# Kernel tuning notes

Measured on AMD Instinct MI355X. Metric: run time of the kernel, lower is better.

Reference implementation:

```python
import jax, jax.numpy as jnp
import numpy as np

HEADS = 8

def group_conv1x1(x, w, heads):
    # x: (B, Cin, H, W); w: (Cout, Cin//heads, 1, 1) grouped 1x1 conv, no bias
    B, Cin, H, W = x.shape
    Cout = w.shape[0]
    xg = x.reshape(B, heads, Cin // heads, H * W)
    wg = w[:, :, 0, 0].reshape(heads, Cout // heads, Cin // heads)
    out = jnp.einsum('hoc,bhcl->bhol', wg, xg)
    return out.reshape(B, Cout, H, W)

def sine_pe(d_model, length):
    # standard transformer sin/cos encoding, laid out as (d_model, length)
    pos = jnp.arange(length, dtype=jnp.float32)
    i = jnp.arange(0, d_model, 2, dtype=jnp.float32)
    div = jnp.exp(-(jnp.log(10000.0)) * i / d_model)
    ang = div[:, None] * pos[None, :]            # (d/2, L)
    pe = jnp.zeros((d_model, length), dtype=jnp.float32)
    pe = pe.at[0::2].set(jnp.sin(ang)).at[1::2].set(jnp.cos(ang))
    return pe

def setup_inputs() -> dict:
    key = jax.random.key(0)
    k0, k1, k2, k3 = jax.random.split(key, 4)
    B, Cin, H, W = 16, 256, 32, 32
    Cout, heads = 256, HEADS
    fan_out = Cout  # kaiming_normal fan_out for 1x1 conv = Cout*1*1
    std = np.sqrt(2.0 / fan_out)
    x = jax.random.normal(k0, (B, Cin, H, W), dtype=jnp.float32)
    wq = jax.random.normal(k1, (Cout, Cin // heads, 1, 1), dtype=jnp.float32) * std
    wk = jax.random.normal(k2, (Cout, Cin // heads, 1, 1), dtype=jnp.float32) * std
    wv = jax.random.normal(k3, (Cout, Cin // heads, 1, 1), dtype=jnp.float32) * std
    return {"x": x, "wq": wq, "wk": wk, "wv": wv}

def reference(x, wq, wk, wv):
    B, Cin, H, W = x.shape
    Cout = wq.shape[0]
    heads = HEADS
    dh = Cout // heads
    L = H * W

    q = group_conv1x1(x, wq, heads)              # (B, Cout, H, W)
    k = group_conv1x1(x, wk, heads)
    v = group_conv1x1(x, wv, heads)

    # sine positional encoding added to keys over flattened spatial positions
    k = k.reshape(B, Cout, L) + sine_pe(Cout, L)[None]

    q = q.reshape(B, heads, dh, L)               # (B, h, dh, L)
    k = k.reshape(B, heads, dh, L)
    v = v.reshape(B, heads, dh, L)

    scores = jnp.einsum('bhdq,bhdk->bhqk', q, k)  # (B, h, L, L) -- no sqrt(d) scaling, as in source
    attn = jax.nn.softmax(scores, axis=-1)
    out = jnp.einsum('bhqk,bhdk->bhdq', attn, v)  # (B, h, dh, L)
    return out.reshape(B, Cout, H, W)
```

## Files before the change

kernel.cpp:

```cpp
#include <hip/hip_runtime.h>

#define LL   1024
#define BHD  128
#define LOG2E 1.44269504088896340736f

typedef unsigned int       uint;
typedef unsigned short     ushort;
typedef unsigned long long ull;

typedef __attribute__((ext_vector_type(8)))  __bf16          bf16x8;
typedef __attribute__((ext_vector_type(8)))  unsigned short  u16x8;
typedef __attribute__((ext_vector_type(2)))  uint            ui32x2;
typedef __attribute__((ext_vector_type(4)))  uint            ui32x4;
typedef __attribute__((ext_vector_type(4)))  float           f32x4;
typedef __attribute__((ext_vector_type(16))) float           f32x16;

static __device__ __forceinline__ ushort f2bf(float f){
  union {float f; uint u;} v; v.f = f;
  uint u = v.u + 0x7fffu + ((v.u >> 16) & 1u);
  return (ushort)(u >> 16);
}
static __device__ __forceinline__ uint pack2(float a, float b){
  return (uint)f2bf(a) | ((uint)f2bf(b) << 16);
}
static __device__ __forceinline__ uint packtrunc(float a, float b){
  union {float f; uint u;} x, y; x.f = a; y.f = b;
  return __builtin_amdgcn_perm(y.u, x.u, 0x07060302u);
}
static __device__ __forceinline__ bf16x8 ld_frag(const ushort* p){
  u16x8 t = *(const u16x8*)p;
  return __builtin_bit_cast(bf16x8, t);
}

static __device__ __forceinline__ bool sniff_is_bf16(const uint* xw, int tid, int* cnt){
  uint w = xw[tid & 255];
  uint e = (w >> 7) & 0xFFu;
  bool hit = (e >= 118u) && (e <= 132u);
  ull b = __ballot(hit);
  if ((tid & 63) == 0) cnt[tid >> 6] = __popcll(b);
  __syncthreads();
  bool r = (cnt[0] + cnt[1] + cnt[2] + cnt[3]) > 128;
  __syncthreads();
  return r;
}

__global__ __launch_bounds__(256) void qkv_kernel(
    const void* __restrict__ xr,
    const void* __restrict__ wqr,
    const void* __restrict__ wkr,
    const void* __restrict__ wvr,
    ushort* __restrict__ Qt, ushort* __restrict__ Kt, ushort* __restrict__ Vt)
{
  const int bh   = blockIdx.x;
  const int lt   = blockIdx.y;
  const int tid  = threadIdx.x;
  const int wave = tid >> 6;
  const int lane = tid & 63;
  const int l16  = lane & 15;
  const int quad = lane >> 4;
  const int lbase = lt * 128;

  __shared__ int cnt[4];
  __shared__ __align__(16) uint xsd[128][20];

  const bool is_bf = sniff_is_bf16((const uint*)xr, tid, cnt);

  {
    const int cp = tid & 15, lg = tid >> 4;
    const size_t rb = (size_t)(bh*32 + 2*cp)*LL + lbase + lg*8;
    uint dw[8];
    if (is_bf){
      u16x8 e = *(const u16x8*)((const ushort*)xr + rb);
      u16x8 o = *(const u16x8*)((const ushort*)xr + rb + LL);
      #pragma unroll
      for (int j = 0; j < 8; ++j) dw[j] = (uint)e[j] | ((uint)o[j] << 16);
    } else {
      const float* xf = (const float*)xr;
      float4 e0 = *(const float4*)(xf + rb);
      float4 e1 = *(const float4*)(xf + rb + 4);
      float4 o0 = *(const float4*)(xf + rb + LL);
      float4 o1 = *(const float4*)(xf + rb + LL + 4);
      dw[0]=pack2(e0.x,o0.x); dw[1]=pack2(e0.y,o0.y);
      dw[2]=pack2(e0.z,o0.z); dw[3]=pack2(e0.w,o0.w);
      dw[4]=pack2(e1.x,o1.x); dw[5]=pack2(e1.y,o1.y);
      dw[6]=pack2(e1.z,o1.z); dw[7]=pack2(e1.w,o1.w);
    }
    #pragma unroll
    for (int j = 0; j < 8; ++j) xsd[lg*8 + j][cp] = dw[j];
  }
  __syncthreads();

  const void* wsrc[3] = {wqr, wkr, wvr};
  bf16x8 bw[3][2];
  #pragma unroll
  for (int p = 0; p < 3; ++p)
    #pragma unroll
    for (int nh = 0; nh < 2; ++nh){
      const int row = (bh & 7)*32 + nh*16 + l16;
      if (is_bf){
        bw[p][nh] = ld_frag((const ushort*)wsrc[p] + (size_t)row*32 + quad*8);
      } else {
        const float* wf = (const float*)wsrc[p] + (size_t)row*32 + quad*8;
        float4 f0 = *(const float4*)wf, f1 = *(const float4*)(wf + 4);
        u16x8 t;
        t[0]=f2bf(f0.x); t[1]=f2bf(f0.y); t[2]=f2bf(f0.z); t[3]=f2bf(f0.w);
        t[4]=f2bf(f1.x); t[5]=f2bf(f1.y); t[6]=f2bf(f1.z); t[7]=f2bf(f1.w);
        bw[p][nh] = __builtin_bit_cast(bf16x8, t);
      }
    }

  bf16x8 ax[2];
  #pragma unroll
  for (int mt = 0; mt < 2; ++mt)
    ax[mt] = __builtin_bit_cast(bf16x8,
               *(const ui32x4*)&xsd[wave*32 + mt*16 + l16][quad*4]);

  const f32x4 z = {0.f,0.f,0.f,0.f};
  f32x4 dq[2][2], dk[2][2], dv[2][2];
  #pragma unroll
  for (int nh = 0; nh < 2; ++nh)
    #pragma unroll
    for (int mt = 0; mt < 2; ++mt){
      dq[nh][mt] = __builtin_amdgcn_mfma_f32_16x16x32_bf16(bw[0][nh], ax[mt], z, 0,0,0);
      dk[nh][mt] = __builtin_amdgcn_mfma_f32_16x16x32_bf16(bw[1][nh], ax[mt], z, 0,0,0);
      dv[mt][nh] = __builtin_amdgcn_mfma_f32_16x16x32_bf16(ax[mt], bw[2][nh], z, 0,0,0);
    }

  const int kt2   = lt*2 + (wave >> 1);
  const size_t bhb = (size_t)bh * 32768;

  #pragma unroll
  for (int nh = 0; nh < 2; ++nh)
    #pragma unroll
    for (int mt = 0; mt < 2; ++mt){
      const int l  = lbase + wave*32 + mt*16 + l16;
      const int d0 = nh*16 + quad*4;
      ui32x2 ww = { pack2(dq[nh][mt][0], dq[nh][mt][1]),
                    pack2(dq[nh][mt][2], dq[nh][mt][3]) };
      *(ui32x2*)&Qt[((size_t)bh*LL + l)*32 + d0] = ww;
    }

  #pragma unroll
  for (int nh = 0; nh < 2; ++nh)
    #pragma unroll
    for (int mt = 0; mt < 2; ++mt){
      const int l  = lbase + wave*32 + mt*16 + l16;
      const int d0 = nh*16 + quad*4;
      const int c0 = (bh & 7)*32 + d0;
      const float fa = __expf(-0.03597789207f * (float)c0);
      const float fb = __expf(-0.03597789207f * (float)(c0 + 2));
      const float aa = fa * (float)l, ab = fb * (float)l;
      const float k0 = (dk[nh][mt][0] + __sinf(aa)) * LOG2E;
      const float k1 = (dk[nh][mt][1] + __cosf(aa)) * LOG2E;
      const float k2 = (dk[nh][mt][2] + __sinf(ab)) * LOG2E;
      const float k3 = (dk[nh][mt][3] + __cosf(ab)) * LOG2E;
      const size_t off = bhb + (size_t)kt2*2048 + (size_t)(wave & 1)*1024
                       + (size_t)nh*512 + (size_t)(quad >> 1)*256
                       + (size_t)(mt*16 + l16)*8 + (quad & 1)*4;
      ui32x2 ww = { pack2(k0, k1), pack2(k2, k3) };
      *(ui32x2*)&Kt[off] = ww;
    }

  #pragma unroll
  for (int mt = 0; mt < 2; ++mt)
    #pragma unroll
    for (int dh = 0; dh < 2; ++dh){
      const size_t off = bhb + (size_t)kt2*2048 + (size_t)((wave*2 + mt) & 3)*512
                       + (size_t)(quad >> 1)*256 + (size_t)(dh*16 + l16)*8
                       + (quad & 1)*4;
      ui32x2 ww = { pack2(dv[mt][dh][0], dv[mt][dh][1]),
                    pack2(dv[mt][dh][2], dv[mt][dh][3]) };
      *(ui32x2*)&Vt[off] = ww;
    }
}

__global__ __launch_bounds__(256, 4) void attn_kernel(
    const void*   __restrict__ xr,
    const ushort* __restrict__ Qt,
    const ushort* __restrict__ Kt,
    const ushort* __restrict__ Vt,
    void* __restrict__ out)
{
  const int bh  = blockIdx.x;
  const int qt  = blockIdx.y;
  const int tid = threadIdx.x;
  const int wave = tid >> 6;
  const int lane = tid & 63;
  const int q32  = lane & 31;
  const int h    = lane >> 5;

  __shared__ int cnt[4];
  const bool is_bf = sniff_is_bf16((const uint*)xr, tid, cnt);

  const int qg = qt*128 + wave*32 + q32;
  const ushort* qrow = Qt + ((size_t)bh*LL + qg)*32;
  bf16x8 bq0 = ld_frag(qrow + h*8);
  bf16x8 bq1 = ld_frag(qrow + 16 + h*8);

  const ushort* kb = Kt + (size_t)bh*32768 + h*256 + q32*8;
  const ushort* vb = Vt + (size_t)bh*32768 + h*256 + q32*8;

  f32x16 O = {};
  float rsum = 0.f;

  for (int kt = 0; kt < 16; ++kt){
    const ushort* kp = kb + kt*2048;
    const ushort* vp = vb + kt*2048;
    bf16x8 k00 = ld_frag(kp);
    bf16x8 k01 = ld_frag(kp + 512);
    bf16x8 k10 = ld_frag(kp + 1024);
    bf16x8 k11 = ld_frag(kp + 1536);
    bf16x8 vf[4];
    vf[0] = ld_frag(vp);
    vf[1] = ld_frag(vp + 512);
    vf[2] = ld_frag(vp + 1024);
    vf[3] = ld_frag(vp + 1536);

    f32x16 st[2];
    { f32x16 zz = {};
      st[0] = __builtin_amdgcn_mfma_f32_32x32x16_bf16(k00, bq0, zz,    0,0,0);
      st[0] = __builtin_amdgcn_mfma_f32_32x32x16_bf16(k01, bq1, st[0], 0,0,0);
      st[1] = __builtin_amdgcn_mfma_f32_32x32x16_bf16(k10, bq0, zz,    0,0,0);
      st[1] = __builtin_amdgcn_mfma_f32_32x32x16_bf16(k11, bq1, st[1], 0,0,0); }

    uint pr[2][8];
    #pragma unroll
    for (int t = 0; t < 2; ++t){
      float ts = 0.f;
      #pragma unroll
      for (int zi = 0; zi < 8; ++zi){
        float p0 = __builtin_amdgcn_exp2f(st[t][2*zi]);
        float p1 = __builtin_amdgcn_exp2f(st[t][2*zi+1]);
        ts += p0 + p1;
        pr[t][zi] = packtrunc(p0, p1);
      }
      rsum += ts;
    }

    #pragma unroll
    for (int c = 0; c < 4; ++c){
      const int t = c >> 1, g0 = 4*(c & 1);
      uint s0 = h ? pr[t][g0+0] : pr[t][g0+2];
      uint s1 = h ? pr[t][g0+1] : pr[t][g0+3];
      uint r0 = (uint)__shfl_xor((int)s0, 32);
      uint r1 = (uint)__shfl_xor((int)s1, 32);
      ui32x4 pb;
      pb[0] = h ? r0 : pr[t][g0+0];
      pb[1] = h ? r1 : pr[t][g0+1];
      pb[2] = h ? pr[t][g0+2] : r0;
      pb[3] = h ? pr[t][g0+3] : r1;
      O = __builtin_amdgcn_mfma_f32_32x32x16_bf16(
            vf[c], __builtin_bit_cast(bf16x8, pb), O, 0,0,0);
    }
  }

  rsum += __shfl_xor(rsum, 32);
  const float inv = 1.f / rsum;

  #pragma unroll
  for (int reg = 0; reg < 16; ++reg){
    const int d = (reg & 3) + 8*(reg >> 2) + 4*h;
    const float v = O[reg] * inv;
    const size_t off = ((size_t)(bh*32 + d))*LL + qg;
    if (is_bf) ((ushort*)out)[off] = f2bf(v);
    else       ((float*)out)[off]  = v;
  }
}

extern "C" void kernel_launch(void* const* d_in, const int* in_sizes, int n_in,
                              void* d_out, int out_size, void* d_ws, size_t ws_size,
                              hipStream_t stream) {
  const void* x  = d_in[0];
  const void* wq = d_in[1];
  const void* wk = d_in[2];
  const void* wv = d_in[3];

  ushort* Qt = (ushort*)d_ws;
  ushort* Kt = Qt + (size_t)BHD * LL * 32;
  ushort* Vt = Kt + (size_t)BHD * LL * 32;

  qkv_kernel <<<dim3(BHD, 8), 256, 0, stream>>>(x, wq, wk, wv, Qt, Kt, Vt);
  attn_kernel<<<dim3(BHD, 8), 256, 0, stream>>>(x, Qt, Kt, Vt, d_out);
}
```

Baseline: 112.6 us.

## Fuse QKV projection into attention kernel with K/V held in LDS

Merges the projection and attention kernels into one launch. Each 512-thread block recomputes the full K and V for one batch-head into about 128KB of shared memory and computes its own Q fragments in registers, so the global round trip of Q/K/V through workspace and the second launch go away. Each wave now handles two 32-query tiles that share K/V fragment loads. The trade-off is that K/V projection is computed twice per head (grid 128x2), and occupancy drops to one large block per CU with only 256 blocks in total.

```diff
diff --git a/kernel.cpp b/kernel.cpp
--- a/kernel.cpp
+++ b/kernel.cpp
@@ -1,8 +1,8 @@
 #include <hip/hip_runtime.h>
 
 #define LL   1024
-#define BHD  128
 #define LOG2E 1.44269504088896340736f
+#define SMEM_BYTES (131072 + 10240 + 32)
 
 typedef unsigned int       uint;
 typedef unsigned short     ushort;
@@ -10,6 +10,7 @@
 
 typedef __attribute__((ext_vector_type(8)))  __bf16          bf16x8;
 typedef __attribute__((ext_vector_type(8)))  unsigned short  u16x8;
+typedef __attribute__((ext_vector_type(4)))  unsigned short  u16x4;
 typedef __attribute__((ext_vector_type(2)))  uint            ui32x2;
 typedef __attribute__((ext_vector_type(4)))  uint            ui32x4;
 typedef __attribute__((ext_vector_type(4)))  float           f32x4;
@@ -31,177 +32,219 @@
   u16x8 t = *(const u16x8*)p;
   return __builtin_bit_cast(bf16x8, t);
 }
-
-static __device__ __forceinline__ bool sniff_is_bf16(const uint* xw, int tid, int* cnt){
-  uint w = xw[tid & 255];
-  uint e = (w >> 7) & 0xFFu;
-  bool hit = (e >= 118u) && (e <= 132u);
-  ull b = __ballot(hit);
-  if ((tid & 63) == 0) cnt[tid >> 6] = __popcll(b);
-  __syncthreads();
-  bool r = (cnt[0] + cnt[1] + cnt[2] + cnt[3]) > 128;
-  __syncthreads();
-  return r;
-}
-
-__global__ __launch_bounds__(256) void qkv_kernel(
+static __device__ __forceinline__ bf16x8 cvt8(const float* p){
+  float4 f0 = *(const float4*)p, f1 = *(const float4*)(p + 4);
+  u16x8 t;
+  t[0]=f2bf(f0.x); t[1]=f2bf(f0.y); t[2]=f2bf(f0.z); t[3]=f2bf(f0.w);
+  t[4]=f2bf(f1.x); t[5]=f2bf(f1.y); t[6]=f2bf(f1.z); t[7]=f2bf(f1.w);
+  return __builtin_bit_cast(bf16x8, t);
+}
+
+static __device__ __forceinline__ void attn_tile(
+    f32x16& O, float& rs, bf16x8 q0, bf16x8 q1,
+    bf16x8 k00, bf16x8 k01, bf16x8 k10, bf16x8 k11,
+    bf16x8 v0, bf16x8 v1, bf16x8 v2, bf16x8 v3, int h)
+{
+  f32x16 zz = {};
+  f32x16 st0 = __builtin_amdgcn_mfma_f32_32x32x16_bf16(k00, q0, zz,  0,0,0);
+  st0        = __builtin_amdgcn_mfma_f32_32x32x16_bf16(k01, q1, st0, 0,0,0);
+  f32x16 st1 = __builtin_amdgcn_mfma_f32_32x32x16_bf16(k10, q0, zz,  0,0,0);
+  st1        = __builtin_amdgcn_mfma_f32_32x32x16_bf16(k11, q1, st1, 0,0,0);
+
+  uint pr0[8], pr1[8];
+  #pragma unroll
+  for (int zi = 0; zi < 8; ++zi){
+    float a0 = __builtin_amdgcn_exp2f(st0[2*zi]);
+    float a1 = __builtin_amdgcn_exp2f(st0[2*zi+1]);
+    float b0 = __builtin_amdgcn_exp2f(st1[2*zi]);
+    float b1 = __builtin_amdgcn_exp2f(st1[2*zi+1]);
+    rs += (a0 + a1) + (b0 + b1);
+    pr0[zi] = packtrunc(a0, a1);
+    pr1[zi] = packtrunc(b0, b1);
+  }
+  const bf16x8 vv[4] = {v0, v1, v2, v3};
+  #pragma unroll
+  for (int c = 0; c < 4; ++c){
+    const uint* pr = (c < 2) ? pr0 : pr1;
+    const int g0 = 4*(c & 1);
+    uint s0 = h ? pr[g0+0] : pr[g0+2];
+    uint s1 = h ? pr[g0+1] : pr[g0+3];
+    uint r0 = (uint)__shfl_xor((int)s0, 32);
+    uint r1 = (uint)__shfl_xor((int)s1, 32);
+    ui32x4 pb;
+    pb[0] = h ? r0 : pr[g0+0];
+    pb[1] = h ? r1 : pr[g0+1];
+    pb[2] = h ? pr[g0+2] : r0;
+    pb[3] = h ? pr[g0+3] : r1;
+    O = __builtin_amdgcn_mfma_f32_32x32x16_bf16(
+          vv[c], __builtin_bit_cast(bf16x8, pb), O, 0,0,0);
+  }
+}
+
+__global__ __launch_bounds__(512, 1) void fused_kernel(
     const void* __restrict__ xr,
     const void* __restrict__ wqr,
     const void* __restrict__ wkr,
     const void* __restrict__ wvr,
-    ushort* __restrict__ Qt, ushort* __restrict__ Kt, ushort* __restrict__ Vt)
+    void* __restrict__ out)
 {
+  extern __shared__ __align__(16) char smem[];
+  ushort* Ks = (ushort*)smem;
+  ushort* Vs = Ks + 32768;
+  uint (*xsd)[20] = (uint (*)[20])(Vs + 32768);
+  int* cnt = (int*)(smem + 131072 + 10240);
+
   const int bh   = blockIdx.x;
-  const int lt   = blockIdx.y;
+  const int qh   = blockIdx.y;
   const int tid  = threadIdx.x;
   const int wave = tid >> 6;
   const int lane = tid & 63;
   const int l16  = lane & 15;
   const int quad = lane >> 4;
-  const int lbase = lt * 128;
-
-  __shared__ int cnt[4];
-  __shared__ __align__(16) uint xsd[128][20];
-
-  const bool is_bf = sniff_is_bf16((const uint*)xr, tid, cnt);
-
+  const int q32  = lane & 31;
+  const int h    = lane >> 5;
+
+  bool is_bf;
   {
-    const int cp = tid & 15, lg = tid >> 4;
-    const size_t rb = (size_t)(bh*32 + 2*cp)*LL + lbase + lg*8;
-    uint dw[8];
+    uint w = ((const uint*)xr)[tid & 255];
+    uint e = (w >> 7) & 0xFFu;
+    ull b = __ballot((e >= 118u) && (e <= 132u));
+    if (lane == 0) cnt[wave] = __popcll(b);
+    __syncthreads();
+    int s = 0;
+    #pragma unroll
+    for (int i = 0; i < 8; ++i) s += cnt[i];
+    is_bf = s > 256;
+  }
+
+  bf16x8 bwk[2], bwv[2], aq[2];
+  #pragma unroll
+  for (int nh = 0; nh < 2; ++nh){
+    const int row = (bh & 7)*32 + nh*16 + l16;
     if (is_bf){
-      u16x8 e = *(const u16x8*)((const ushort*)xr + rb);
-      u16x8 o = *(const u16x8*)((const ushort*)xr + rb + LL);
-      #pragma unroll
-      for (int j = 0; j < 8; ++j) dw[j] = (uint)e[j] | ((uint)o[j] << 16);
+      bwk[nh] = ld_frag((const ushort*)wkr + (size_t)row*32 + quad*8);
+      bwv[nh] = ld_frag((const ushort*)wvr + (size_t)row*32 + quad*8);
     } else {
-      const float* xf = (const float*)xr;
-      float4 e0 = *(const float4*)(xf + rb);
-      float4 e1 = *(const float4*)(xf + rb + 4);
-      float4 o0 = *(const float4*)(xf + rb + LL);
-      float4 o1 = *(const float4*)(xf + rb + LL + 4);
-      dw[0]=pack2(e0.x,o0.x); dw[1]=pack2(e0.y,o0.y);
-      dw[2]=pack2(e0.z,o0.z); dw[3]=pack2(e0.w,o0.w);
-      dw[4]=pack2(e1.x,o1.x); dw[5]=pack2(e1.y,o1.y);
-      dw[6]=pack2(e1.z,o1.z); dw[7]=pack2(e1.w,o1.w);
-    }
-    #pragma unroll
-    for (int j = 0; j < 8; ++j) xsd[lg*8 + j][cp] = dw[j];
-  }
-  __syncthreads();
-
-  const void* wsrc[3] = {wqr, wkr, wvr};
-  bf16x8 bw[3][2];
-  #pragma unroll
-  for (int p = 0; p < 3; ++p)
+      bwk[nh] = cvt8((const float*)wkr + (size_t)row*32 + quad*8);
+      bwv[nh] = cvt8((const float*)wvr + (size_t)row*32 + quad*8);
+    }
+  }
+  {
+    const int row = (bh & 7)*32 + q32;
+    if (is_bf){
+      aq[0] = ld_frag((const ushort*)wqr + (size_t)row*32 + h*8);
+      aq[1] = ld_frag((const ushort*)wqr + (size_t)row*32 + 16 + h*8);
+    } else {
+      aq[0] = cvt8((const float*)wqr + (size_t)row*32 + h*8);
+      aq[1] = cvt8((const float*)wqr + (size_t)row*32 + 16 + h*8);
+    }
+  }
+
+  const int myoc = 4*qh + (wave >> 1);
+  bf16x8 bq[2][2];
+
+  for (int lc = 0; lc < 8; ++lc){
+    if (lc) __syncthreads();
+    {
+      const int cp = tid & 15, lg = tid >> 4;
+      const size_t rb = (size_t)(bh*32 + 2*cp)*LL + (size_t)lc*128 + lg*4;
+      uint dw[4];
+      if (is_bf){
+        u16x4 e = *(const u16x4*)((const ushort*)xr + rb);
+        u16x4 o = *(const u16x4*)((const ushort*)xr + rb + LL);
+        #pragma unroll
+        for (int j = 0; j < 4; ++j) dw[j] = (uint)e[j] | ((uint)o[j] << 16);
+      } else {
+        const float* xf = (const float*)xr;
+        float4 e0 = *(const float4*)(xf + rb);
+        float4 o0 = *(const float4*)(xf + rb + LL);
+        dw[0]=pack2(e0.x,o0.x); dw[1]=pack2(e0.y,o0.y);
+        dw[2]=pack2(e0.z,o0.z); dw[3]=pack2(e0.w,o0.w);
+      }
+      #pragma unroll
+      for (int j = 0; j < 4; ++j) xsd[lg*4 + j][cp] = dw[j];
+    }
+    __syncthreads();
+
+    bf16x8 ax = __builtin_bit_cast(bf16x8,
+                  *(const ui32x4*)&xsd[wave*16 + l16][quad*4]);
+
+    const f32x4 z = {0.f,0.f,0.f,0.f};
+    f32x4 dk[2], dv[2];
     #pragma unroll
     for (int nh = 0; nh < 2; ++nh){
-      const int row = (bh & 7)*32 + nh*16 + l16;
-      if (is_bf){
-        bw[p][nh] = ld_frag((const ushort*)wsrc[p] + (size_t)row*32 + quad*8);
-      } else {
-        const float* wf = (const float*)wsrc[p] + (size_t)row*32 + quad*8;
-        float4 f0 = *(const float4*)wf, f1 = *(const float4*)(wf + 4);
-        u16x8 t;
-        t[0]=f2bf(f0.x); t[1]=f2bf(f0.y); t[2]=f2bf(f0.z); t[3]=f2bf(f0.w);
-        t[4]=f2bf(f1.x); t[5]=f2bf(f1.y); t[6]=f2bf(f1.z); t[7]=f2bf(f1.w);
-        bw[p][nh] = __builtin_bit_cast(bf16x8, t);
-      }
-    }
-
-  bf16x8 ax[2];
-  #pragma unroll
-  for (int mt = 0; mt < 2; ++mt)
-    ax[mt] = __builtin_bit_cast(bf16x8,
-               *(const ui32x4*)&xsd[wave*32 + mt*16 + l16][quad*4]);
-
-  const f32x4 z = {0.f,0.f,0.f,0.f};
-  f32x4 dq[2][2], dk[2][2], dv[2][2];
-  #pragma unroll
-  for (int nh = 0; nh < 2; ++nh)
-    #pragma unroll
-    for (int mt = 0; mt < 2; ++mt){
-      dq[nh][mt] = __builtin_amdgcn_mfma_f32_16x16x32_bf16(bw[0][nh], ax[mt], z, 0,0,0);
-      dk[nh][mt] = __builtin_amdgcn_mfma_f32_16x16x32_bf16(bw[1][nh], ax[mt], z, 0,0,0);
-      dv[mt][nh] = __builtin_amdgcn_mfma_f32_16x16x32_bf16(ax[mt], bw[2][nh], z, 0,0,0);
-    }
-
-  const int kt2   = lt*2 + (wave >> 1);
-  const size_t bhb = (size_t)bh * 32768;
-
-  #pragma unroll
-  for (int nh = 0; nh < 2; ++nh)
-    #pragma unroll
-    for (int mt = 0; mt < 2; ++mt){
-      const int l  = lbase + wave*32 + mt*16 + l16;
-      const int d0 = nh*16 + quad*4;
-      ui32x2 ww = { pack2(dq[nh][mt][0], dq[nh][mt][1]),
-                    pack2(dq[nh][mt][2], dq[nh][mt][3]) };
-      *(ui32x2*)&Qt[((size_t)bh*LL + l)*32 + d0] = ww;
-    }
-
-  #pragma unroll
-  for (int nh = 0; nh < 2; ++nh)
-    #pragma unroll
-    for (int mt = 0; mt < 2; ++mt){
-      const int l  = lbase + wave*32 + mt*16 + l16;
-      const int d0 = nh*16 + quad*4;
-      const int c0 = (bh & 7)*32 + d0;
-      const float fa = __expf(-0.03597789207f * (float)c0);
-      const float fb = __expf(-0.03597789207f * (float)(c0 + 2));
-      const float aa = fa * (float)l, ab = fb * (float)l;
-      const float k0 = (dk[nh][mt][0] + __sinf(aa)) * LOG2E;
-      const float k1 = (dk[nh][mt][1] + __cosf(aa)) * LOG2E;
-      const float k2 = (dk[nh][mt][2] + __sinf(ab)) * LOG2E;
-      const float k3 = (dk[nh][mt][3] + __cosf(ab)) * LOG2E;
-      const size_t off = bhb + (size_t)kt2*2048 + (size_t)(wave & 1)*1024
-                       + (size_t)nh*512 + (size_t)(quad >> 1)*256
-                       + (size_t)(mt*16 + l16)*8 + (quad & 1)*4;
-      ui32x2 ww = { pack2(k0, k1), pack2(k2, k3) };
-      *(ui32x2*)&Kt[off] = ww;
-    }
-
-  #pragma unroll
-  for (int mt = 0; mt < 2; ++mt)
-    #pragma unroll
-    for (int dh = 0; dh < 2; ++dh){
-      const size_t off = bhb + (size_t)kt2*2048 + (size_t)((wave*2 + mt) & 3)*512
-                       + (size_t)(quad >> 1)*256 + (size_t)(dh*16 + l16)*8
-                       + (quad & 1)*4;
-      ui32x2 ww = { pack2(dv[mt][dh][0], dv[mt][dh][1]),
-                    pack2(dv[mt][dh][2], dv[mt][dh][3]) };
-      *(ui32x2*)&Vt[off] = ww;
-    }
-}
-
-__global__ __launch_bounds__(256, 4) void attn_kernel(
-    const void*   __restrict__ xr,
-    const ushort* __restrict__ Qt,
-    const ushort* __restrict__ Kt,
-    const ushort* __restrict__ Vt,
-    void* __restrict__ out)
-{
-  const int bh  = blockIdx.x;
-  const int qt  = blockIdx.y;
-  const int tid = threadIdx.x;
-  const int wave = tid >> 6;
-  const int lane = tid & 63;
-  const int q32  = lane & 31;
-  const int h    = lane >> 5;
-
-  __shared__ int cnt[4];
-  const bool is_bf = sniff_is_bf16((const uint*)xr, tid, cnt);
-
-  const int qg = qt*128 + wave*32 + q32;
-  const ushort* qrow = Qt + ((size_t)bh*LL + qg)*32;
-  bf16x8 bq0 = ld_frag(qrow + h*8);
-  bf16x8 bq1 = ld_frag(qrow + 16 + h*8);
-
-  const ushort* kb = Kt + (size_t)bh*32768 + h*256 + q32*8;
-  const ushort* vb = Vt + (size_t)bh*32768 + h*256 + q32*8;
-
-  f32x16 O = {};
-  float rsum = 0.f;
+      dk[nh] = __builtin_amdgcn_mfma_f32_16x16x32_bf16(bwk[nh], ax, z, 0,0,0);
+      dv[nh] = __builtin_amdgcn_mfma_f32_16x16x32_bf16(ax, bwv[nh], z, 0,0,0);
+    }
+
+    {
+      const int kl = lc*128 + wave*16 + l16;
+      const int kbase = (kl >> 6)*2048 + ((kl >> 5) & 1)*1024
+                      + (quad >> 1)*256 + (kl & 31)*8 + (quad & 1)*4;
+      #pragma unroll
+      for (int nh = 0; nh < 2; ++nh){
+        const int d0 = nh*16 + quad*4;
+        const int c0 = (bh & 7)*32 + d0;
+        const float fa = __expf(-0.03597789207f * (float)c0);
+        const float fb = __expf(-0.03597789207f * (float)(c0 + 2));
+        const float aa = fa * (float)kl, ab = fb * (float)kl;
+        const float k0 = (dk[nh][0] + __sinf(aa)) * LOG2E;
+        const float k1 = (dk[nh][1] + __cosf(aa)) * LOG2E;
+        const float k2 = (dk[nh][2] + __sinf(ab)) * LOG2E;
+        const float k3 = (dk[nh][3] + __cosf(ab)) * LOG2E;
+        ui32x2 ww = { pack2(k0, k1), pack2(k2, k3) };
+        *(ui32x2*)&Ks[kbase + nh*512] = ww;
+      }
+    }
+    {
+      const int vl = lc*128 + wave*16 + quad*4;
+      const int vbase = (vl >> 6)*2048 + (wave & 3)*512
+                      + (quad >> 1)*256 + (quad & 1)*4;
+      #pragma unroll
+      for (int nh = 0; nh < 2; ++nh){
+        ui32x2 ww = { pack2(dv[nh][0], dv[nh][1]),
+                      pack2(dv[nh][2], dv[nh][3]) };
+        *(ui32x2*)&Vs[vbase + (nh*16 + l16)*8] = ww;
+      }
+    }
+
+    if (lc == myoc){
+      const int xbase = (wave & 1)*64;
+      #pragma unroll
+      for (int qt2 = 0; qt2 < 2; ++qt2){
+        const int xrow = xbase + qt2*32 + q32;
+        bf16x8 bxl = __builtin_bit_cast(bf16x8, *(const ui32x4*)&xsd[xrow][h*4]);
+        bf16x8 bxh = __builtin_bit_cast(bf16x8, *(const ui32x4*)&xsd[xrow][8 + h*4]);
+        f32x16 zz = {};
+        f32x16 dq = __builtin_amdgcn_mfma_f32_32x32x16_bf16(aq[0], bxl, zz, 0,0,0);
+        dq        = __builtin_amdgcn_mfma_f32_32x32x16_bf16(aq[1], bxh, dq, 0,0,0);
+        uint prq[8];
+        #pragma unroll
+        for (int zi = 0; zi < 8; ++zi) prq[zi] = pack2(dq[2*zi], dq[2*zi+1]);
+        #pragma unroll
+        for (int hf = 0; hf < 2; ++hf){
+          const int g0 = 4*hf;
+          uint s0 = h ? prq[g0+0] : prq[g0+2];
+          uint s1 = h ? prq[g0+1] : prq[g0+3];
+          uint r0 = (uint)__shfl_xor((int)s0, 32);
+          uint r1 = (uint)__shfl_xor((int)s1, 32);
+          ui32x4 pb;
+          pb[0] = h ? r0 : prq[g0+0];
+          pb[1] = h ? r1 : prq[g0+1];
+          pb[2] = h ? prq[g0+2] : r0;
+          pb[3] = h ? prq[g0+3] : r1;
+          bq[qt2][hf] = __builtin_bit_cast(bf16x8, pb);
+        }
+      }
+    }
+  }
+  __syncthreads();
+
+  const ushort* kb = Ks + h*256 + q32*8;
+  const ushort* vb = Vs + h*256 + q32*8;
+
+  f32x16 O0 = {}, O1 = {};
+  float rs0 = 0.f, rs1 = 0.f;
 
   for (int kt = 0; kt < 16; ++kt){
     const ushort* kp = kb + kt*2048;
@@ -210,75 +253,43 @@
     bf16x8 k01 = ld_frag(kp + 512);
     bf16x8 k10 = ld_frag(kp + 1024);
     bf16x8 k11 = ld_frag(kp + 1536);
-    bf16x8 vf[4];
-    vf[0] = ld_frag(vp);
-    vf[1] = ld_frag(vp + 512);
-    vf[2] = ld_frag(vp + 1024);
-    vf[3] = ld_frag(vp + 1536);
-
-    f32x16 st[2];
-    { f32x16 zz = {};
-      st[0] = __builtin_amdgcn_mfma_f32_32x32x16_bf16(k00, bq0, zz,    0,0,0);
-      st[0] = __builtin_amdgcn_mfma_f32_32x32x16_bf16(k01, bq1, st[0], 0,0,0);
-      st[1] = __builtin_amdgcn_mfma_f32_32x32x16_bf16(k10, bq0, zz,    0,0,0);
-      st[1] = __builtin_amdgcn_mfma_f32_32x32x16_bf16(k11, bq1, st[1], 0,0,0); }
-
-    uint pr[2][8];
-    #pragma unroll
-    for (int t = 0; t < 2; ++t){
-      float ts = 0.f;
-      #pragma unroll
-      for (int zi = 0; zi < 8; ++zi){
-        float p0 = __builtin_amdgcn_exp2f(st[t][2*zi]);
-        float p1 = __builtin_amdgcn_exp2f(st[t][2*zi+1]);
-        ts += p0 + p1;
-        pr[t][zi] = packtrunc(p0, p1);
-      }
-      rsum += ts;
-    }
-
-    #pragma unroll
-    for (int c = 0; c < 4; ++c){
-      const int t = c >> 1, g0 = 4*(c & 1);
-      uint s0 = h ? pr[t][g0+0] : pr[t][g0+2];
-      uint s1 = h ? pr[t][g0+1] : pr[t][g0+3];
-      uint r0 = (uint)__shfl_xor((int)s0, 32);
-      uint r1 = (uint)__shfl_xor((int)s1, 32);
-      ui32x4 pb;
-      pb[0] = h ? r0 : pr[t][g0+0];
-      pb[1] = h ? r1 : pr[t][g0+1];
-      pb[2] = h ? pr[t][g0+2] : r0;
-      pb[3] = h ? pr[t][g0+3] : r1;
-      O = __builtin_amdgcn_mfma_f32_32x32x16_bf16(
-            vf[c], __builtin_bit_cast(bf16x8, pb), O, 0,0,0);
-    }
-  }
-
-  rsum += __shfl_xor(rsum, 32);
-  const float inv = 1.f / rsum;
-
+    bf16x8 v0  = ld_frag(vp);
+    bf16x8 v1  = ld_frag(vp + 512);
+    bf16x8 v2  = ld_frag(vp + 1024);
+    bf16x8 v3  = ld_frag(vp + 1536);
+    attn_tile(O0, rs0, bq[0][0], bq[0][1], k00,k01,k10,k11, v0,v1,v2,v3, h);
+    attn_tile(O1, rs1, bq[1][0], bq[1][1], k00,k01,k10,k11, v0,v1,v2,v3, h);
+  }
+
+  rs0 += __shfl_xor(rs0, 32);
+  rs1 += __shfl_xor(rs1, 32);
+  const float inv0 = 1.f / rs0, inv1 = 1.f / rs1;
+
+  const int qg0 = qh*512 + wave*64 + q32;
   #pragma unroll
   for (int reg = 0; reg < 16; ++reg){
     const int d = (reg & 3) + 8*(reg >> 2) + 4*h;
-    const float v = O[reg] * inv;
-    const size_t off = ((size_t)(bh*32 + d))*LL + qg;
-    if (is_bf) ((ushort*)out)[off] = f2bf(v);
-    else       ((float*)out)[off]  = v;
+    const size_t o0 = ((size_t)(bh*32 + d))*LL + qg0;
+    if (is_bf){
+      ((ushort*)out)[o0]      = f2bf(O0[reg] * inv0);
+      ((ushort*)out)[o0 + 32] = f2bf(O1[reg] * inv1);
+    } else {
+      ((float*)out)[o0]      = O0[reg] * inv0;
+      ((float*)out)[o0 + 32] = O1[reg] * inv1;
+    }
   }
 }
 
 extern "C" void kernel_launch(void* const* d_in, const int* in_sizes, int n_in,
                               void* d_out, int out_size, void* d_ws, size_t ws_size,
                               hipStream_t stream) {
-  const void* x  = d_in[0];
-  const void* wq = d_in[1];
-  const void* wk = d_in[2];
-  const void* wv = d_in[3];
-
-  ushort* Qt = (ushort*)d_ws;
-  ushort* Kt = Qt + (size_t)BHD * LL * 32;
-  ushort* Vt = Kt + (size_t)BHD * LL * 32;
-
-  qkv_kernel <<<dim3(BHD, 8), 256, 0, stream>>>(x, wq, wk, wv, Qt, Kt, Vt);
-  attn_kernel<<<dim3(BHD, 8), 256, 0, stream>>>(x, Qt, Kt, Vt, d_out);
-}
+  (void)d_ws; (void)ws_size; (void)in_sizes; (void)n_in; (void)out_size;
+  static bool inited = false;
+  if (!inited){
+    hipFuncSetAttribute(reinterpret_cast<const void*>(fused_kernel),
+                        hipFuncAttributeMaxDynamicSharedMemorySize, SMEM_BYTES);
+    inited = true;
+  }
+  fused_kernel<<<dim3(128, 2), 512, SMEM_BYTES, stream>>>(
+      d_in[0], d_in[1], d_in[2], d_in[3], d_out);
+}
```

After: 105.5 us. -6.3%, faster.
